# Performance work log

Hardware: AMD Instinct MI355X
Metric: run time of the kernel (lower is better)

## Reference

```python
import jax, jax.numpy as jnp
import numpy as np

N0, N1, N2, N3 = 600000, 100000, 10000, 1000
E0, E1, E2 = 1000000, 100000, 10000
DIN, DH, DOUT = 128, 256, 47


def _glorot(k, fan_in, fan_out):
    s = np.sqrt(2.0 / (fan_in + fan_out)).astype(np.float32)
    return jax.random.normal(k, (fan_in, fan_out), jnp.float32) * s


def setup_inputs() -> dict:
    key = jax.random.key(0)
    ks = jax.random.split(key, 13)
    return {
        "x": jax.random.normal(ks[0], (N0, DIN), jnp.float32),
        "src0": jax.random.randint(ks[1], (E0,), 0, N0, jnp.int32),
        "dst0": jax.random.randint(ks[2], (E0,), 0, N1, jnp.int32),
        "src1": jax.random.randint(ks[3], (E1,), 0, N1, jnp.int32),
        "dst1": jax.random.randint(ks[4], (E1,), 0, N2, jnp.int32),
        "src2": jax.random.randint(ks[5], (E2,), 0, N2, jnp.int32),
        "dst2": jax.random.randint(ks[6], (E2,), 0, N3, jnp.int32),
        "Wl0": _glorot(ks[7], DIN, DH), "Wr0": _glorot(ks[8], DIN, DH),
        "b0": jnp.zeros((DH,), jnp.float32),
        "Wl1": _glorot(ks[9], DH, DH), "Wr1": _glorot(ks[10], DH, DH),
        "b1": jnp.zeros((DH,), jnp.float32),
        "Wl2": _glorot(ks[11], DH, DOUT), "Wr2": _glorot(ks[12], DH, DOUT),
        "b2": jnp.zeros((DOUT,), jnp.float32),
        "size1": N1, "size2": N2, "size3": N3,
    }


def _sage_conv(x, src, dst, n_tgt, Wl, Wr, b):
    # PyG SAGEConv (mean aggr, root_weight=True, bias in lin_l) on a bipartite
    # sampled subgraph: x_src = x (all frontier nodes), x_tgt = x[:n_tgt].
    msgs = x[src]                                   # [E, Din] gather
    agg = jax.ops.segment_sum(msgs, dst, num_segments=n_tgt)
    cnt = jax.ops.segment_sum(jnp.ones((dst.shape[0],), x.dtype), dst,
                              num_segments=n_tgt)
    mean = agg / jnp.maximum(cnt, 1.0)[:, None]     # [n_tgt, Din]
    return mean @ Wl + b + x[:n_tgt] @ Wr           # [n_tgt, Dout]


def reference(x, src0, dst0, src1, dst1, src2, dst2,
              Wl0, Wr0, b0, Wl1, Wr1, b1, Wl2, Wr2, b2,
              size1, size2, size3):
    # layer 0
    h = jax.nn.relu(_sage_conv(x, src0, dst0, size1, Wl0, Wr0, b0))
    # dropout(p=0.5) is identity in eval mode
    # layer 1
    h = jax.nn.relu(_sage_conv(h, src1, dst1, size2, Wl1, Wr1, b1))
    # layer 2 (no relu/dropout)
    h = _sage_conv(h, src2, dst2, size3, Wl2, Wr2, b2)
    return jax.nn.log_softmax(h, axis=-1)           # [size3, out_channels]
```

## Files before the change

### kernel.cpp

```cpp
#include <hip/hip_runtime.h>
#include <hip/hip_bf16.h>
#include <cstdint>
#include <cstddef>
#include <cmath>

#define N0C 600000
#define N1C 100000
#define N2C 10000
#define N3C 1000
#define E0C 1000000
#define E1C 100000
#define E2C 10000

typedef unsigned short u16;
typedef unsigned int u32;
typedef __attribute__((ext_vector_type(8))) short bf16x8;
typedef __attribute__((ext_vector_type(4))) float f32x4;

__device__ __forceinline__ u16 f2b(float x) {
  u32 u = __builtin_bit_cast(u32, x);
  u32 r = (u + 0x7fffu + ((u >> 16) & 1u)) >> 16;
  return (u16)r;
}
__device__ __forceinline__ u16 f2b_hw(float x) {
  __hip_bfloat16 h = __float2bfloat16(x);
  u16 r;
  __builtin_memcpy(&r, &h, 2);
  return r;
}
__device__ __forceinline__ float b2f(u16 h) {
  u32 u = ((u32)h) << 16;
  return __builtin_bit_cast(float, u);
}

__global__ __launch_bounds__(256) void hist3(
    const int* __restrict__ d0, const int* __restrict__ d1,
    const int* __restrict__ d2, int* __restrict__ c0, int* __restrict__ c1,
    int* __restrict__ c2) {
  int i = blockIdx.x * blockDim.x + threadIdx.x;
  if (i < E0C) atomicAdd(&c0[d0[i]], 1);
  else if (i < E0C + E1C) atomicAdd(&c1[d1[i - E0C]], 1);
  else if (i < E0C + E1C + E2C) atomicAdd(&c2[d2[i - E0C - E1C]], 1);
}

__global__ __launch_bounds__(256) void scan_block3(
    int* __restrict__ c0, int* __restrict__ c1, int* __restrict__ c2,
    int* __restrict__ p0, int* __restrict__ p1, int* __restrict__ p2) {
  __shared__ int sdata[256];
  const int b = blockIdx.x;
  int* data; int n; int* partials; int lb;
  if (b < 98)       { data = c0; n = N1C; partials = p0; lb = b; }
  else if (b < 108) { data = c1; n = N2C; partials = p1; lb = b - 98; }
  else              { data = c2; n = N3C; partials = p2; lb = b - 108; }
  const int t = threadIdx.x;
  const int idx = lb * 1024 + t * 4;
  int v[4];
  int sum = 0;
#pragma unroll
  for (int k = 0; k < 4; k++) {
    int x = (idx + k < n) ? data[idx + k] : 0;
    v[k] = x; sum += x;
  }
  sdata[t] = sum;
  __syncthreads();
  for (int off = 1; off < 256; off <<= 1) {
    int x = (t >= off) ? sdata[t - off] : 0;
    __syncthreads();
    sdata[t] += x;
    __syncthreads();
  }
  int run = (t > 0) ? sdata[t - 1] : 0;
#pragma unroll
  for (int k = 0; k < 4; k++) {
    run += v[k];
    if (idx + k < n) data[idx + k] = run;
  }
  if (t == 255) partials[lb] = sdata[255];
}

__global__ __launch_bounds__(128) void scan_partials3(
    int* __restrict__ p0, int* __restrict__ p1, int* __restrict__ p2) {
  __shared__ int sdata[128];
  int* p; int nb;
  if (blockIdx.x == 0)      { p = p0; nb = 98; }
  else if (blockIdx.x == 1) { p = p1; nb = 10; }
  else                      { p = p2; nb = 1; }
  const int t = threadIdx.x;
  sdata[t] = (t < nb) ? p[t] : 0;
  __syncthreads();
  for (int off = 1; off < 128; off <<= 1) {
    int x = (t >= off) ? sdata[t - off] : 0;
    __syncthreads();
    sdata[t] += x;
    __syncthreads();
  }
  int ex = (t > 0) ? sdata[t - 1] : 0;
  if (t < nb) p[t] = ex;
}

__global__ __launch_bounds__(256) void addoff3(
    const int* __restrict__ c0, const int* __restrict__ c1,
    const int* __restrict__ c2, const int* __restrict__ p0,
    const int* __restrict__ p1, const int* __restrict__ p2,
    int* __restrict__ o0, int* __restrict__ o1, int* __restrict__ o2) {
  int i = blockIdx.x * blockDim.x + threadIdx.x;
  if (i < N1C) {
    o0[i + 1] = c0[i] + p0[i >> 10];
    if (i == 0) o0[0] = 0;
  } else if (i < N1C + N2C) {
    int j = i - N1C;
    o1[j + 1] = c1[j] + p1[j >> 10];
    if (j == 0) o1[0] = 0;
  } else if (i < N1C + N2C + N3C) {
    int j = i - N1C - N2C;
    o2[j + 1] = c2[j] + p2[j >> 10];
    if (j == 0) o2[0] = 0;
  }
}

__global__ __launch_bounds__(256) void fill3(
    const int* __restrict__ s0, const int* __restrict__ d0,
    const int* __restrict__ s1, const int* __restrict__ d1,
    const int* __restrict__ s2, const int* __restrict__ d2,
    const int* __restrict__ o0, const int* __restrict__ o1,
    const int* __restrict__ o2, int* __restrict__ u0, int* __restrict__ u1,
    int* __restrict__ u2, int* __restrict__ e0, int* __restrict__ e1,
    int* __restrict__ e2) {
  int i = blockIdx.x * blockDim.x + threadIdx.x;
  if (i < E0C) {
    int d = d0[i]; int p = atomicAdd(&u0[d], 1); e0[o0[d] + p] = s0[i];
  } else if (i < E0C + E1C) {
    int j = i - E0C;
    int d = d1[j]; int p = atomicAdd(&u1[d], 1); e1[o1[d] + p] = s1[j];
  } else if (i < E0C + E1C + E2C) {
    int j = i - E0C - E1C;
    int d = d2[j]; int p = atomicAdd(&u2[d], 1); e2[o2[d] + p] = s2[j];
  }
}

__global__ __launch_bounds__(256) void cvt_wt2(
    const float* __restrict__ Wl0, const float* __restrict__ Wr0,
    const float* __restrict__ Wl1, const float* __restrict__ Wr1,
    u16* __restrict__ Wt0, u16* __restrict__ Wt1) {
  int idx = blockIdx.x * blockDim.x + threadIdx.x;
  if (idx < 256 * 256) {
    int n = idx >> 8, k = idx & 255;
    float v = (k < 128) ? Wl0[(size_t)k * 256 + n] : Wr0[(size_t)(k - 128) * 256 + n];
    Wt0[idx] = f2b(v);
  } else if (idx < 256 * 256 + 256 * 512) {
    int j = idx - 256 * 256;
    int n = j >> 9, k = j & 511;
    float v = (k < 256) ? Wl1[(size_t)k * 256 + n] : Wr1[(size_t)(k - 256) * 256 + n];
    Wt1[j] = f2b(v);
  }
}

__global__ __launch_bounds__(256) void gather128_f32(
    const float* __restrict__ X, const int* __restrict__ off,
    const int* __restrict__ esrc, int Nt, u16* __restrict__ mean) {
  int w = (blockIdx.x * blockDim.x + threadIdx.x) >> 6;
  int lane = threadIdx.x & 63;
  if (w >= Nt) return;
  const int half = lane >> 5, l32 = lane & 31;
  int s = off[w], e = off[w + 1];
  float a0 = 0.f, a1 = 0.f, a2 = 0.f, a3 = 0.f;
  int j = s;
  for (; j + 3 < e; j += 4) {
    float4 v0 = *(const float4*)(X + (size_t)esrc[j + half] * 128 + l32 * 4);
    float4 v1 = *(const float4*)(X + (size_t)esrc[j + 2 + half] * 128 + l32 * 4);
    a0 += v0.x + v1.x; a1 += v0.y + v1.y;
    a2 += v0.z + v1.z; a3 += v0.w + v1.w;
  }
  for (; j + 1 < e; j += 2) {
    float4 v = *(const float4*)(X + (size_t)esrc[j + half] * 128 + l32 * 4);
    a0 += v.x; a1 += v.y; a2 += v.z; a3 += v.w;
  }
  if (j < e && half == 0) {
    float4 v = *(const float4*)(X + (size_t)esrc[j] * 128 + l32 * 4);
    a0 += v.x; a1 += v.y; a2 += v.z; a3 += v.w;
  }
  a0 += __shfl_xor(a0, 32, 64);
  a1 += __shfl_xor(a1, 32, 64);
  a2 += __shfl_xor(a2, 32, 64);
  a3 += __shfl_xor(a3, 32, 64);
  if (half == 0) {
    float inv = 1.0f / fmaxf((float)(e - s), 1.0f);
    uint2 pk;
    pk.x = ((u32)f2b(a1 * inv) << 16) | (u32)f2b(a0 * inv);
    pk.y = ((u32)f2b(a3 * inv) << 16) | (u32)f2b(a2 * inv);
    *(uint2*)(mean + (size_t)w * 128 + l32 * 4) = pk;
  }
}

__global__ __launch_bounds__(256) void gather256_bf16(
    const u16* __restrict__ X, const int* __restrict__ off,
    const int* __restrict__ esrc, int Nt, u16* __restrict__ mean) {
  int w = (blockIdx.x * blockDim.x + threadIdx.x) >> 6;
  int lane = threadIdx.x & 63;
  if (w >= Nt) return;
  int s = off[w], e = off[w + 1];
  float a0 = 0.f, a1 = 0.f, a2 = 0.f, a3 = 0.f;
  int j = s;
  for (; j + 3 < e; j += 4) {
    ushort4 v0 = *(const ushort4*)(X + (size_t)esrc[j + 0] * 256 + lane * 4);
    ushort4 v1 = *(const ushort4*)(X + (size_t)esrc[j + 1] * 256 + lane * 4);
    ushort4 v2 = *(const ushort4*)(X + (size_t)esrc[j + 2] * 256 + lane * 4);
    ushort4 v3 = *(const ushort4*)(X + (size_t)esrc[j + 3] * 256 + lane * 4);
    a0 += b2f(v0.x) + b2f(v1.x) + b2f(v2.x) + b2f(v3.x);
    a1 += b2f(v0.y) + b2f(v1.y) + b2f(v2.y) + b2f(v3.y);
    a2 += b2f(v0.z) + b2f(v1.z) + b2f(v2.z) + b2f(v3.z);
    a3 += b2f(v0.w) + b2f(v1.w) + b2f(v2.w) + b2f(v3.w);
  }
  for (; j < e; j++) {
    ushort4 v0 = *(const ushort4*)(X + (size_t)esrc[j] * 256 + lane * 4);
    a0 += b2f(v0.x); a1 += b2f(v0.y); a2 += b2f(v0.z); a3 += b2f(v0.w);
  }
  float inv = 1.0f / fmaxf((float)(e - s), 1.0f);
  ushort4 o;
  o.x = f2b(a0 * inv); o.y = f2b(a1 * inv); o.z = f2b(a2 * inv); o.w = f2b(a3 * inv);
  *(ushort4*)(mean + (size_t)w * 256 + lane * 4) = o;
}

__global__ __launch_bounds__(256) void gemm_mfma_l0(
    const u16* __restrict__ A1, const float* __restrict__ A2,
    const u16* __restrict__ Wt, const float* __restrict__ bias,
    u16* __restrict__ C, int M) {
  const int tid = threadIdx.x;
  const int wave = tid >> 6, lane = tid & 63;
  const int lr = lane & 15, quad = lane >> 4;
  const int wr = wave >> 1, wc = wave & 1;
  const int rowBase = blockIdx.x * 128 + wr * 64;
  const int colBase = blockIdx.y * 128 + wc * 64;

  f32x4 acc[4][4] = {};

  int rrow[4];
#pragma unroll
  for (int mt = 0; mt < 4; mt++) {
    int r = rowBase + mt * 16 + lr;
    if (r >= M) r = M - 1;
    rrow[mt] = r;
  }
  const u16* wrow[4];
  float bs[4];
#pragma unroll
  for (int nt = 0; nt < 4; nt++) {
    int n = colBase + nt * 16 + lr;
    wrow[nt] = Wt + (size_t)n * 256;
    bs[nt] = bias[n];
  }

#pragma unroll
  for (int kt = 0; kt < 128; kt += 32) {
    bf16x8 af[4], bfr[4];
#pragma unroll
    for (int mt = 0; mt < 4; mt++)
      af[mt] = *(const bf16x8*)(A1 + (size_t)rrow[mt] * 128 + kt + quad * 8);
#pragma unroll
    for (int nt = 0; nt < 4; nt++)
      bfr[nt] = *(const bf16x8*)(wrow[nt] + kt + quad * 8);
#pragma unroll
    for (int mt = 0; mt < 4; mt++)
#pragma unroll
      for (int nt = 0; nt < 4; nt++)
        acc[mt][nt] = __builtin_amdgcn_mfma_f32_16x16x32_bf16(
            af[mt], bfr[nt], acc[mt][nt], 0, 0, 0);
  }
#pragma unroll
  for (int kt = 0; kt < 128; kt += 32) {
    bf16x8 af[4], bfr[4];
#pragma unroll
    for (int mt = 0; mt < 4; mt++) {
      const float* s = A2 + (size_t)rrow[mt] * 128 + kt + quad * 8;
      float4 v0 = *(const float4*)s;
      float4 v1 = *(const float4*)(s + 4);
      bf16x8 t;
      t[0] = (short)f2b_hw(v0.x); t[1] = (short)f2b_hw(v0.y);
      t[2] = (short)f2b_hw(v0.z); t[3] = (short)f2b_hw(v0.w);
      t[4] = (short)f2b_hw(v1.x); t[5] = (short)f2b_hw(v1.y);
      t[6] = (short)f2b_hw(v1.z); t[7] = (short)f2b_hw(v1.w);
      af[mt] = t;
    }
#pragma unroll
    for (int nt = 0; nt < 4; nt++)
      bfr[nt] = *(const bf16x8*)(wrow[nt] + 128 + kt + quad * 8);
#pragma unroll
    for (int mt = 0; mt < 4; mt++)
#pragma unroll
      for (int nt = 0; nt < 4; nt++)
        acc[mt][nt] = __builtin_amdgcn_mfma_f32_16x16x32_bf16(
            af[mt], bfr[nt], acc[mt][nt], 0, 0, 0);
  }

#pragma unroll
  for (int mt = 0; mt < 4; mt++) {
#pragma unroll
    for (int reg = 0; reg < 4; reg++) {
      int row = rowBase + mt * 16 + quad * 4 + reg;
      if (row < M) {
#pragma unroll
        for (int nt = 0; nt < 4; nt++) {
          float v = fmaxf(acc[mt][nt][reg] + bs[nt], 0.f);
          C[(size_t)row * 256 + colBase + nt * 16 + lr] = f2b(v);
        }
      }
    }
  }
}

__global__ __launch_bounds__(256) void gemm_mfma(
    const u16* __restrict__ A1, const u16* __restrict__ A2, int Kh,
    const u16* __restrict__ Wt, const float* __restrict__ bias,
    u16* __restrict__ C, int M, int do_relu) {
  const int tid = threadIdx.x;
  const int wave = tid >> 6, lane = tid & 63;
  const int lr = lane & 15, quad = lane >> 4;
  const int wr = wave >> 1, wc = wave & 1;
  const int rowBase = blockIdx.x * 128 + wr * 64;
  const int colBase = blockIdx.y * 128 + wc * 64;
  const int Ktot = 2 * Kh;

  f32x4 acc[4][4] = {};

  size_t aoff[4];
#pragma unroll
  for (int mt = 0; mt < 4; mt++) {
    int r = rowBase + mt * 16 + lr;
    if (r >= M) r = M - 1;
    aoff[mt] = (size_t)r * Kh;
  }
  const u16* wrow[4];
  float bs[4];
#pragma unroll
  for (int nt = 0; nt < 4; nt++) {
    int n = colBase + nt * 16 + lr;
    wrow[nt] = Wt + (size_t)n * Ktot;
    bs[nt] = bias[n];
  }

#pragma unroll
  for (int half = 0; half < 2; half++) {
    const u16* Asrc = half ? A2 : A1;
    const int kb = half * Kh;
    for (int kt = 0; kt < Kh; kt += 32) {
      bf16x8 af[4], bfr[4];
#pragma unroll
      for (int mt = 0; mt < 4; mt++)
        af[mt] = *(const bf16x8*)(Asrc + aoff[mt] + kt + quad * 8);
#pragma unroll
      for (int nt = 0; nt < 4; nt++)
        bfr[nt] = *(const bf16x8*)(wrow[nt] + kb + kt + quad * 8);
#pragma unroll
      for (int mt = 0; mt < 4; mt++)
#pragma unroll
        for (int nt = 0; nt < 4; nt++)
          acc[mt][nt] = __builtin_amdgcn_mfma_f32_16x16x32_bf16(
              af[mt], bfr[nt], acc[mt][nt], 0, 0, 0);
    }
  }

#pragma unroll
  for (int mt = 0; mt < 4; mt++) {
#pragma unroll
    for (int reg = 0; reg < 4; reg++) {
      int row = rowBase + mt * 16 + quad * 4 + reg;
      if (row < M) {
#pragma unroll
        for (int nt = 0; nt < 4; nt++) {
          float v = acc[mt][nt][reg] + bs[nt];
          if (do_relu) v = fmaxf(v, 0.f);
          C[(size_t)row * 256 + colBase + nt * 16 + lr] = f2b(v);
        }
      }
    }
  }
}

__global__ __launch_bounds__(64) void l2_fused(
    const u16* __restrict__ h2, const int* __restrict__ off,
    const int* __restrict__ esrc, const float* __restrict__ Wl2,
    const float* __restrict__ Wr2, const float* __restrict__ b2,
    float* __restrict__ out) {
  __shared__ float arow[512];
  const int i = blockIdx.x;
  const int lane = threadIdx.x;

  int s = off[i], e = off[i + 1];
  float a0 = 0.f, a1 = 0.f, a2 = 0.f, a3 = 0.f;
  int j = s;
  for (; j + 3 < e; j += 4) {
    ushort4 v0 = *(const ushort4*)(h2 + (size_t)esrc[j + 0] * 256 + lane * 4);
    ushort4 v1 = *(const ushort4*)(h2 + (size_t)esrc[j + 1] * 256 + lane * 4);
    ushort4 v2 = *(const ushort4*)(h2 + (size_t)esrc[j + 2] * 256 + lane * 4);
    ushort4 v3 = *(const ushort4*)(h2 + (size_t)esrc[j + 3] * 256 + lane * 4);
    a0 += b2f(v0.x) + b2f(v1.x) + b2f(v2.x) + b2f(v3.x);
    a1 += b2f(v0.y) + b2f(v1.y) + b2f(v2.y) + b2f(v3.y);
    a2 += b2f(v0.z) + b2f(v1.z) + b2f(v2.z) + b2f(v3.z);
    a3 += b2f(v0.w) + b2f(v1.w) + b2f(v2.w) + b2f(v3.w);
  }
  for (; j < e; j++) {
    ushort4 v0 = *(const ushort4*)(h2 + (size_t)esrc[j] * 256 + lane * 4);
    a0 += b2f(v0.x); a1 += b2f(v0.y); a2 += b2f(v0.z); a3 += b2f(v0.w);
  }
  float inv = 1.0f / fmaxf((float)(e - s), 1.0f);
  arow[lane * 4 + 0] = a0 * inv;
  arow[lane * 4 + 1] = a1 * inv;
  arow[lane * 4 + 2] = a2 * inv;
  arow[lane * 4 + 3] = a3 * inv;
  ushort4 r = *(const ushort4*)(h2 + (size_t)i * 256 + lane * 4);
  arow[256 + lane * 4 + 0] = b2f(r.x);
  arow[256 + lane * 4 + 1] = b2f(r.y);
  arow[256 + lane * 4 + 2] = b2f(r.z);
  arow[256 + lane * 4 + 3] = b2f(r.w);
  __syncthreads();

  float acc = 0.0f;
  if (lane < 47) {
    acc = b2[lane];
#pragma unroll 4
    for (int k = 0; k < 256; k++) acc += arow[k] * Wl2[k * 47 + lane];
#pragma unroll 4
    for (int k = 0; k < 256; k++) acc += arow[256 + k] * Wr2[k * 47 + lane];
  }
  float v = (lane < 47) ? acc : -INFINITY;
#pragma unroll
  for (int off2 = 32; off2 >= 1; off2 >>= 1) v = fmaxf(v, __shfl_xor(v, off2, 64));
  float e2 = (lane < 47) ? expf(acc - v) : 0.0f;
  float s2 = e2;
#pragma unroll
  for (int off2 = 32; off2 >= 1; off2 >>= 1) s2 += __shfl_xor(s2, off2, 64);
  if (lane < 47) out[(size_t)i * 47 + lane] = acc - v - logf(s2);
}

extern "C" void kernel_launch(void* const* d_in, const int* in_sizes, int n_in,
                              void* d_out, int out_size, void* d_ws, size_t ws_size,
                              hipStream_t stream) {
  (void)in_sizes; (void)n_in; (void)out_size; (void)ws_size;
  const float* x   = (const float*)d_in[0];
  const int* src0  = (const int*)d_in[1];
  const int* dst0  = (const int*)d_in[2];
  const int* src1  = (const int*)d_in[3];
  const int* dst1  = (const int*)d_in[4];
  const int* src2  = (const int*)d_in[5];
  const int* dst2  = (const int*)d_in[6];
  const float* Wl0 = (const float*)d_in[7];
  const float* Wr0 = (const float*)d_in[8];
  const float* b0  = (const float*)d_in[9];
  const float* Wl1 = (const float*)d_in[10];
  const float* Wr1 = (const float*)d_in[11];
  const float* b1  = (const float*)d_in[12];
  const float* Wl2 = (const float*)d_in[13];
  const float* Wr2 = (const float*)d_in[14];
  const float* b2  = (const float*)d_in[15];

  char* p = (char*)d_ws;
  u16* mean0 = (u16*)p; p += (size_t)N1C * 128 * 2;
  u16* h1    = (u16*)p; p += (size_t)N1C * 256 * 2;
  u16* mean1 = (u16*)p; p += (size_t)N2C * 256 * 2;
  u16* h2    = (u16*)p; p += (size_t)N2C * 256 * 2;
  u16* Wt0   = (u16*)p; p += (size_t)256 * 256 * 2;
  u16* Wt1   = (u16*)p; p += (size_t)256 * 512 * 2;
  int* cnt0  = (int*)p;
  int* cur0  = cnt0 + 100000;
  int* cnt1  = cur0 + 100000;
  int* cur1  = cnt1 + 10000;
  int* cnt2  = cur1 + 10000;
  int* cur2  = cnt2 + 1000;
  int* off0  = cur2 + 1000 + 48;
  int* off1  = off0 + 100096;
  int* off2  = off1 + 10112;
  int* part0 = off2 + 1088;
  int* part1 = part0 + 128;
  int* part2 = part1 + 128;
  int* esrc0 = part2 + 128;
  int* esrc1 = esrc0 + 1000000;
  int* esrc2 = esrc1 + 100000;
  float* out = (float*)d_out;

  hipMemsetAsync(cnt0, 0, (size_t)222000 * 4, stream);
  hist3<<<(E0C + E1C + E2C + 255) / 256, 256, 0, stream>>>(
      dst0, dst1, dst2, cnt0, cnt1, cnt2);
  scan_block3<<<109, 256, 0, stream>>>(cnt0, cnt1, cnt2, part0, part1, part2);
  scan_partials3<<<3, 128, 0, stream>>>(part0, part1, part2);
  addoff3<<<(N1C + N2C + N3C + 255) / 256, 256, 0, stream>>>(
      cnt0, cnt1, cnt2, part0, part1, part2, off0, off1, off2);
  fill3<<<(E0C + E1C + E2C + 255) / 256, 256, 0, stream>>>(
      src0, dst0, src1, dst1, src2, dst2, off0, off1, off2,
      cur0, cur1, cur2, esrc0, esrc1, esrc2);

  cvt_wt2<<<(256 * 256 + 256 * 512 + 255) / 256, 256, 0, stream>>>(
      Wl0, Wr0, Wl1, Wr1, Wt0, Wt1);

  gather128_f32<<<N1C / 4, 256, 0, stream>>>(x, off0, esrc0, N1C, mean0);
  gemm_mfma_l0<<<dim3(782, 2), 256, 0, stream>>>(mean0, x, Wt0, b0, h1, N1C);

  gather256_bf16<<<N2C / 4, 256, 0, stream>>>(h1, off1, esrc1, N2C, mean1);
  gemm_mfma<<<dim3(79, 2), 256, 0, stream>>>(mean1, h1, 256, Wt1, b1, h2, N2C, 1);

  l2_fused<<<N3C, 64, 0, stream>>>(h2, off2, esrc2, Wl2, Wr2, b2, out);
}
```

Measured before the change: 732.3 us.

## Compute layer-0 outputs only for nodes consumed by layer 1

Marks the layer-1 nodes that are actually read: the sources of layer-1 edges plus the first N2 root rows. It then scans those flags into a compact list and index map. The layer-0 gather and GEMM run only over the listed nodes and write h1 in compacted order, and layer-1 edge sources are remapped through the index map. This removes the aggregation and matmul for layer-0 nodes that nothing reads. The cost is an extra scan, one more level of indirection, and grids still sized for the full node count, whose surplus blocks exit early.

Measured after the change: 696.7 us. 4.9% less time.

```diff
diff --git a/kernel.cpp b/kernel.cpp
--- a/kernel.cpp
+++ b/kernel.cpp
@@ -35,23 +35,33 @@
 
 __global__ __launch_bounds__(256) void hist3(
     const int* __restrict__ d0, const int* __restrict__ d1,
-    const int* __restrict__ d2, int* __restrict__ c0, int* __restrict__ c1,
-    int* __restrict__ c2) {
+    const int* __restrict__ d2, const int* __restrict__ s1,
+    int* __restrict__ c0, int* __restrict__ c1, int* __restrict__ c2,
+    int* __restrict__ f) {
   int i = blockIdx.x * blockDim.x + threadIdx.x;
-  if (i < E0C) atomicAdd(&c0[d0[i]], 1);
-  else if (i < E0C + E1C) atomicAdd(&c1[d1[i - E0C]], 1);
-  else if (i < E0C + E1C + E2C) atomicAdd(&c2[d2[i - E0C - E1C]], 1);
+  if (i < E0C) {
+    atomicAdd(&c0[d0[i]], 1);
+    if (i < N2C) f[i] = 1;
+  } else if (i < E0C + E1C) {
+    int j = i - E0C;
+    atomicAdd(&c1[d1[j]], 1);
+    f[s1[j]] = 1;
+  } else if (i < E0C + E1C + E2C) {
+    atomicAdd(&c2[d2[i - E0C - E1C]], 1);
+  }
 }
 
 __global__ __launch_bounds__(256) void scan_block3(
     int* __restrict__ c0, int* __restrict__ c1, int* __restrict__ c2,
-    int* __restrict__ p0, int* __restrict__ p1, int* __restrict__ p2) {
+    int* __restrict__ f, int* __restrict__ p0, int* __restrict__ p1,
+    int* __restrict__ p2, int* __restrict__ pf) {
   __shared__ int sdata[256];
   const int b = blockIdx.x;
   int* data; int n; int* partials; int lb;
   if (b < 98)       { data = c0; n = N1C; partials = p0; lb = b; }
   else if (b < 108) { data = c1; n = N2C; partials = p1; lb = b - 98; }
-  else              { data = c2; n = N3C; partials = p2; lb = b - 108; }
+  else if (b < 109) { data = c2; n = N3C; partials = p2; lb = b - 108; }
+  else              { data = f;  n = N1C; partials = pf; lb = b - 109; }
   const int t = threadIdx.x;
   const int idx = lb * 1024 + t * 4;
   int v[4];
@@ -79,12 +89,14 @@
 }
 
 __global__ __launch_bounds__(128) void scan_partials3(
-    int* __restrict__ p0, int* __restrict__ p1, int* __restrict__ p2) {
+    int* __restrict__ p0, int* __restrict__ p1, int* __restrict__ p2,
+    int* __restrict__ pf) {
   __shared__ int sdata[128];
   int* p; int nb;
   if (blockIdx.x == 0)      { p = p0; nb = 98; }
   else if (blockIdx.x == 1) { p = p1; nb = 10; }
-  else                      { p = p2; nb = 1; }
+  else if (blockIdx.x == 2) { p = p2; nb = 1; }
+  else                      { p = pf; nb = 98; }
   const int t = threadIdx.x;
   sdata[t] = (t < nb) ? p[t] : 0;
   __syncthreads();
@@ -102,11 +114,19 @@
     const int* __restrict__ c0, const int* __restrict__ c1,
     const int* __restrict__ c2, const int* __restrict__ p0,
     const int* __restrict__ p1, const int* __restrict__ p2,
-    int* __restrict__ o0, int* __restrict__ o1, int* __restrict__ o2) {
+    int* __restrict__ o0, int* __restrict__ o1, int* __restrict__ o2,
+    const int* __restrict__ f, const int* __restrict__ pf,
+    int* __restrict__ cidx, int* __restrict__ list,
+    int* __restrict__ cnt_need) {
   int i = blockIdx.x * blockDim.x + threadIdx.x;
   if (i < N1C) {
     o0[i + 1] = c0[i] + p0[i >> 10];
     if (i == 0) o0[0] = 0;
+    int F = f[i] + pf[i >> 10];
+    int prev = (i > 0) ? (f[i - 1] + pf[(i - 1) >> 10]) : 0;
+    cidx[i] = prev;
+    if (F > prev) list[prev] = i;
+    if (i == N1C - 1) cnt_need[0] = F;
   } else if (i < N1C + N2C) {
     int j = i - N1C;
     o1[j + 1] = c1[j] + p1[j >> 10];
@@ -125,13 +145,14 @@
     const int* __restrict__ o0, const int* __restrict__ o1,
     const int* __restrict__ o2, int* __restrict__ u0, int* __restrict__ u1,
     int* __restrict__ u2, int* __restrict__ e0, int* __restrict__ e1,
-    int* __restrict__ e2) {
+    int* __restrict__ e2, const int* __restrict__ cidx) {
   int i = blockIdx.x * blockDim.x + threadIdx.x;
   if (i < E0C) {
     int d = d0[i]; int p = atomicAdd(&u0[d], 1); e0[o0[d] + p] = s0[i];
   } else if (i < E0C + E1C) {
     int j = i - E0C;
-    int d = d1[j]; int p = atomicAdd(&u1[d], 1); e1[o1[d] + p] = s1[j];
+    int d = d1[j]; int p = atomicAdd(&u1[d], 1);
+    e1[o1[d] + p] = cidx[s1[j]];
   } else if (i < E0C + E1C + E2C) {
     int j = i - E0C - E1C;
     int d = d2[j]; int p = atomicAdd(&u2[d], 1); e2[o2[d] + p] = s2[j];
@@ -157,12 +178,14 @@
 
 __global__ __launch_bounds__(256) void gather128_f32(
     const float* __restrict__ X, const int* __restrict__ off,
-    const int* __restrict__ esrc, int Nt, u16* __restrict__ mean) {
+    const int* __restrict__ esrc, const int* __restrict__ list,
+    const int* __restrict__ cnt_need, u16* __restrict__ mean) {
   int w = (blockIdx.x * blockDim.x + threadIdx.x) >> 6;
   int lane = threadIdx.x & 63;
-  if (w >= Nt) return;
+  if (w >= cnt_need[0]) return;
+  const int node = list[w];
   const int half = lane >> 5, l32 = lane & 31;
-  int s = off[w], e = off[w + 1];
+  int s = off[node], e = off[node + 1];
   float a0 = 0.f, a1 = 0.f, a2 = 0.f, a3 = 0.f;
   int j = s;
   for (; j + 3 < e; j += 4) {
@@ -223,8 +246,11 @@
 
 __global__ __launch_bounds__(256) void gemm_mfma_l0(
     const u16* __restrict__ A1, const float* __restrict__ A2,
+    const int* __restrict__ list, const int* __restrict__ cnt_need,
     const u16* __restrict__ Wt, const float* __restrict__ bias,
-    u16* __restrict__ C, int M) {
+    u16* __restrict__ C) {
+  const int M = cnt_need[0];
+  if ((int)blockIdx.x * 128 >= M) return;
   const int tid = threadIdx.x;
   const int wave = tid >> 6, lane = tid & 63;
   const int lr = lane & 15, quad = lane >> 4;
@@ -234,12 +260,13 @@
 
   f32x4 acc[4][4] = {};
 
-  int rrow[4];
+  int rrow[4], node[4];
 #pragma unroll
   for (int mt = 0; mt < 4; mt++) {
     int r = rowBase + mt * 16 + lr;
     if (r >= M) r = M - 1;
     rrow[mt] = r;
+    node[mt] = list[r];
   }
   const u16* wrow[4];
   float bs[4];
@@ -271,7 +298,7 @@
     bf16x8 af[4], bfr[4];
 #pragma unroll
     for (int mt = 0; mt < 4; mt++) {
-      const float* s = A2 + (size_t)rrow[mt] * 128 + kt + quad * 8;
+      const float* s = A2 + (size_t)node[mt] * 128 + kt + quad * 8;
       float4 v0 = *(const float4*)s;
       float4 v1 = *(const float4*)(s + 4);
       bf16x8 t;
@@ -466,33 +493,41 @@
   int* cur1  = cnt1 + 10000;
   int* cnt2  = cur1 + 10000;
   int* cur2  = cnt2 + 1000;
-  int* off0  = cur2 + 1000 + 48;
+  int* f     = cur2 + 1000;
+  int* off0  = f + 100000 + 48;
   int* off1  = off0 + 100096;
   int* off2  = off1 + 10112;
   int* part0 = off2 + 1088;
   int* part1 = part0 + 128;
   int* part2 = part1 + 128;
-  int* esrc0 = part2 + 128;
+  int* pf    = part2 + 128;
+  int* cntN  = pf + 128;
+  int* cidx  = cntN + 64;
+  int* list  = cidx + 100000;
+  int* esrc0 = list + 100000;
   int* esrc1 = esrc0 + 1000000;
   int* esrc2 = esrc1 + 100000;
   float* out = (float*)d_out;
 
-  hipMemsetAsync(cnt0, 0, (size_t)222000 * 4, stream);
+  hipMemsetAsync(cnt0, 0, (size_t)322000 * 4, stream);
   hist3<<<(E0C + E1C + E2C + 255) / 256, 256, 0, stream>>>(
-      dst0, dst1, dst2, cnt0, cnt1, cnt2);
-  scan_block3<<<109, 256, 0, stream>>>(cnt0, cnt1, cnt2, part0, part1, part2);
-  scan_partials3<<<3, 128, 0, stream>>>(part0, part1, part2);
+      dst0, dst1, dst2, src1, cnt0, cnt1, cnt2, f);
+  scan_block3<<<207, 256, 0, stream>>>(cnt0, cnt1, cnt2, f,
+                                       part0, part1, part2, pf);
+  scan_partials3<<<4, 128, 0, stream>>>(part0, part1, part2, pf);
   addoff3<<<(N1C + N2C + N3C + 255) / 256, 256, 0, stream>>>(
-      cnt0, cnt1, cnt2, part0, part1, part2, off0, off1, off2);
+      cnt0, cnt1, cnt2, part0, part1, part2, off0, off1, off2,
+      f, pf, cidx, list, cntN);
   fill3<<<(E0C + E1C + E2C + 255) / 256, 256, 0, stream>>>(
       src0, dst0, src1, dst1, src2, dst2, off0, off1, off2,
-      cur0, cur1, cur2, esrc0, esrc1, esrc2);
+      cur0, cur1, cur2, esrc0, esrc1, esrc2, cidx);
 
   cvt_wt2<<<(256 * 256 + 256 * 512 + 255) / 256, 256, 0, stream>>>(
       Wl0, Wr0, Wl1, Wr1, Wt0, Wt1);
 
-  gather128_f32<<<N1C / 4, 256, 0, stream>>>(x, off0, esrc0, N1C, mean0);
-  gemm_mfma_l0<<<dim3(782, 2), 256, 0, stream>>>(mean0, x, Wt0, b0, h1, N1C);
+  gather128_f32<<<N1C / 4, 256, 0, stream>>>(x, off0, esrc0, list, cntN, mean0);
+  gemm_mfma_l0<<<dim3(782, 2), 256, 0, stream>>>(mean0, x, list, cntN,
+                                                 Wt0, b0, h1);
 
   gather256_bf16<<<N2C / 4, 256, 0, stream>>>(h1, off1, esrc1, N2C, mean1);
   gemm_mfma<<<dim3(79, 2), 256, 0, stream>>>(mean1, h1, 256, Wt1, b1, h2, N2C, 1);
```
